# Kernel optimization log

Hardware: AMD Instinct MI355X
Metric: run time of the kernel (lower is better)

The kernel has to match this reference:

```python
import jax, jax.numpy as jnp
import numpy as np

B, N, C = 4, 2048, 1024
H = 16
D = C // H  # head dim = 64

def setup_inputs() -> dict:
    key = jax.random.key(0)
    k1, k2, k3 = jax.random.split(key, 3)
    x = jax.random.normal(k1, (B, N, C), dtype=jnp.float32)
    w_attn = jax.random.normal(k2, (C, 3 * C), dtype=jnp.float32) * (C ** -0.5)
    w_proj = jax.random.normal(k3, (C, C), dtype=jnp.float32) * (C ** -0.5)
    return {"x": x, "w_attn": w_attn, "w_proj": w_proj}

def reference(x, w_attn, w_proj):
    # fused QKV projection (bias=False)
    qkv = jnp.einsum('bnc,cf->bnf', x, w_attn)            # [B,N,3C]
    q, k, v = jnp.split(qkv, 3, axis=-1)                  # each [B,N,C]
    # [B,H,N,D]
    q = q.reshape(B, N, H, D).transpose(0, 2, 1, 3)
    k = k.reshape(B, N, H, D).transpose(0, 2, 1, 3)
    v = v.reshape(B, N, H, D).transpose(0, 2, 1, 3)
    # scaled dot-product attention, non-causal, no mask, dropout_p=0
    scale = 1.0 / jnp.sqrt(jnp.asarray(D, dtype=q.dtype))
    scores = jnp.einsum('bhqd,bhkd->bhqk', q, k) * scale  # [B,H,N,N]
    attn = jax.nn.softmax(scores, axis=-1)
    y = jnp.einsum('bhqk,bhkd->bhqd', attn, v)            # [B,H,N,D]
    y = y.transpose(0, 2, 1, 3).reshape(B, N, C)
    # output projection (bias=False); resid dropout is identity at p=0
    return jnp.einsum('bnc,co->bno', y, w_proj)
```

## Files before the change

### kernel.cpp

```cpp
#include <hip/hip_runtime.h>
#include <hip/hip_bf16.h>

typedef __hip_bfloat16 bf16;
typedef short short8 __attribute__((ext_vector_type(8)));
typedef float f32x4 __attribute__((ext_vector_type(4)));
typedef float f32x16 __attribute__((ext_vector_type(16)));

#define GLOBAL_AS __attribute__((address_space(1)))
#define LDS_AS __attribute__((address_space(3)))

__device__ inline unsigned short f2bf(float x) {
    union { float f; unsigned u; } v; v.f = x;
    unsigned r = v.u + 0x7fffu + ((v.u >> 16) & 1u);
    return (unsigned short)(r >> 16);
}

__device__ inline unsigned pkbf(float a, float b) {
    float2 f; f.x = a; f.y = b;
    union { __hip_bfloat162 h; unsigned u; } c;
    c.h = __float22bfloat162_rn(f);
    return c.u;
}

__device__ inline float fast_exp2(float x) {
#if __has_builtin(__builtin_amdgcn_exp2f)
    return __builtin_amdgcn_exp2f(x);
#else
    return exp2f(x);
#endif
}

__device__ inline void async16(const void* g, void* l) {
    __builtin_amdgcn_global_load_lds((const GLOBAL_AS void*)g, (LDS_AS void*)l, 16, 0, 0);
}


__global__ __launch_bounds__(256) void cvt_f32_bf16(const float* __restrict__ in,
                                                    unsigned short* __restrict__ out, int n4) {
    int i = blockIdx.x * 256 + threadIdx.x;
    if (i < n4) {
        float4 v = ((const float4*)in)[i];
        ushort4 o;
        o.x = f2bf(v.x); o.y = f2bf(v.y); o.z = f2bf(v.z); o.w = f2bf(v.w);
        ((ushort4*)out)[i] = o;
    }
}

__global__ __launch_bounds__(256) void transpose_bf16(const float* __restrict__ in,
                                                      unsigned short* __restrict__ out,
                                                      int R, int Cc) {
    __shared__ float s[32][33];
    int tx = threadIdx.x & 31, ty = threadIdx.x >> 5;
    int c0 = blockIdx.x * 32, r0 = blockIdx.y * 32;
#pragma unroll
    for (int i = 0; i < 4; i++)
        s[ty + i * 8][tx] = in[(size_t)(r0 + ty + i * 8) * Cc + c0 + tx];
    __syncthreads();
#pragma unroll
    for (int i = 0; i < 4; i++)
        out[(size_t)(c0 + ty + i * 8) * R + r0 + tx] = f2bf(s[tx][ty + i * 8]);
}


template <int MODE>
__global__ __launch_bounds__(256) void gemm_bf16(const bf16* __restrict__ A,
                                                 const bf16* __restrict__ Bt,
                                                 unsigned short* __restrict__ outQ,
                                                 unsigned short* __restrict__ outK,
                                                 unsigned short* __restrict__ outV,
                                                 float* __restrict__ outF, float qscale) {
    const int KD = 1024;
    __shared__ __align__(16) char smem[34816];
    bf16* sA = (bf16*)smem;
    bf16* sB = (bf16*)(smem + 16384);
    const int t = threadIdx.x;
    const int w = t >> 6, lane = t & 63, l15 = lane & 15, qd = lane >> 4;
    const int bn = blockIdx.x, bm = blockIdx.y;
    const int wm = (w >> 1) * 64, wn = (w & 1) * 64;
    const int sw = l15 & 7;

    f32x4 acc[4][4];
#pragma unroll
    for (int i = 0; i < 4; i++)
#pragma unroll
        for (int j = 0; j < 4; j++) acc[i][j] = (f32x4){0.f, 0.f, 0.f, 0.f};

    const int rsub = lane >> 3;
    const int csrc = ((lane & 7) ^ rsub) << 3;
    const bf16* Ab = A + (size_t)(bm * 128 + w * 32 + rsub) * KD + csrc;
    const bf16* Bb = Bt + (size_t)(bn * 128 + w * 32 + rsub) * KD + csrc;
    bf16* sAw = sA + (w * 32) * 64;
    bf16* sBw = sB + (w * 32) * 64;

    for (int kt = 0; kt < 16; ++kt) {
#pragma unroll
        for (int j = 0; j < 4; ++j) {
            async16(Ab + (size_t)(j * 8) * KD + kt * 64, sAw + j * 512);
            async16(Bb + (size_t)(j * 8) * KD + kt * 64, sBw + j * 512);
        }
        __syncthreads();
#pragma unroll
        for (int ks = 0; ks < 2; ++ks) {
            const int cphys = (((ks * 4 + qd) ^ sw) << 3);
            short8 af[4], bfv[4];
#pragma unroll
            for (int mi = 0; mi < 4; mi++)
                af[mi] = *(const short8*)&sA[(wm + mi * 16 + l15) * 64 + cphys];
#pragma unroll
            for (int ni = 0; ni < 4; ni++)
                bfv[ni] = *(const short8*)&sB[(wn + ni * 16 + l15) * 64 + cphys];
#pragma unroll
            for (int mi = 0; mi < 4; mi++)
#pragma unroll
                for (int ni = 0; ni < 4; ni++)
                    acc[mi][ni] = __builtin_amdgcn_mfma_f32_16x16x32_bf16(af[mi], bfv[ni],
                                                                          acc[mi][ni], 0, 0, 0);
        }
        __syncthreads();
    }

    if (MODE == 0) {
        unsigned short* sC = (unsigned short*)smem;
        const int part = bn >> 3;
        const int hb = (bn & 7) * 2;
        if (part < 2) {
            const float sc = (part == 0) ? qscale : 1.0f;
            unsigned short* dst = (part == 0) ? outQ : outK;
#pragma unroll
            for (int mi = 0; mi < 4; mi++)
#pragma unroll
                for (int ni = 0; ni < 4; ni++)
#pragma unroll
                    for (int r = 0; r < 4; r++)
                        sC[(wm + mi * 16 + qd * 4 + r) * 136 + wn + ni * 16 + l15] =
                            f2bf(acc[mi][ni][r] * sc);
            __syncthreads();
#pragma unroll
            for (int i = 0; i < 8; i++) {
                const int j = t + i * 256;
                const int row = j >> 4, c16 = j & 15;
                uint4 v = *(const uint4*)&sC[row * 136 + c16 * 8];
                const int m = bm * 128 + row;
                const int b = m >> 11, ns = m & 2047;
                const int h = hb + (c16 >> 3);
                const int dd = (c16 & 7) * 8;
                *(uint4*)&dst[((size_t)(b * 16 + h) * 2048 + ns) * 64 + dd] = v;
            }
        } else {
#pragma unroll
            for (int ni = 0; ni < 4; ni++)
#pragma unroll
                for (int mi = 0; mi < 4; mi++) {
                    uint2 pk;
                    pk.x = (unsigned)f2bf(acc[mi][ni][0]) | ((unsigned)f2bf(acc[mi][ni][1]) << 16);
                    pk.y = (unsigned)f2bf(acc[mi][ni][2]) | ((unsigned)f2bf(acc[mi][ni][3]) << 16);
                    *(uint2*)&sC[(wn + ni * 16 + l15) * 136 + wm + mi * 16 + qd * 4] = pk;
                }
            __syncthreads();
            const int m0b = bm * 128;
            const int b = m0b >> 11, ns0 = m0b & 2047;
#pragma unroll
            for (int i = 0; i < 8; i++) {
                const int j = t + i * 256;
                const int f = j >> 4, tc = j & 15;
                uint4 v = *(const uint4*)&sC[f * 136 + tc * 8];
                const int h = hb + (f >> 6), dd = f & 63;
                *(uint4*)&outV[((size_t)(b * 16 + h) * 64 + dd) * 2048 + ns0 + tc * 8] = v;
            }
        }
    } else {
        float* sF = (float*)smem;
#pragma unroll
        for (int pass = 0; pass < 2; ++pass) {
            if (pass) __syncthreads();
            if ((wm >> 6) == pass) {
#pragma unroll
                for (int mi = 0; mi < 4; mi++)
#pragma unroll
                    for (int ni = 0; ni < 4; ni++)
#pragma unroll
                        for (int r = 0; r < 4; r++)
                            sF[(mi * 16 + qd * 4 + r) * 132 + wn + ni * 16 + l15] =
                                acc[mi][ni][r];
            }
            __syncthreads();
#pragma unroll
            for (int i = 0; i < 8; i++) {
                const int j = t + i * 256;
                const int row = j >> 5, c4 = j & 31;
                float4 v = *(const float4*)&sF[row * 132 + c4 * 4];
                *(float4*)&outF[(size_t)(bm * 128 + pass * 64 + row) * 1024 + bn * 128 +
                                c4 * 4] = v;
            }
        }
    }
}


__global__ __launch_bounds__(256) void attn_kernel(const bf16* __restrict__ Q,
                                                   const bf16* __restrict__ K,
                                                   const bf16* __restrict__ Vt,
                                                   bf16* __restrict__ Y) {
    const int blk = blockIdx.x;
    const int bh = (blk & 7) * 8 + (blk >> 7);
    const int qt = (blk >> 3) & 15;
    const int b = bh >> 4, h16 = bh & 15;
    const int t = threadIdx.x, w = t >> 6, lane = t & 63;
    const int c = lane & 31, hl = lane >> 5;
    const int sw = c & 7;

    __shared__ __align__(16) char smem[32768];
    bf16* sK = (bf16*)smem;
    bf16* sVt = (bf16*)(smem + 16384);
    bf16* sO = (bf16*)smem;

    const size_t bhbase = (size_t)bh * 2048 * 64;

    short8 qf[4];
#pragma unroll
    for (int kc = 0; kc < 4; kc++)
        qf[kc] = *(const short8*)(Q + bhbase + (size_t)(qt * 128 + w * 32 + c) * 64 +
                                  kc * 16 + hl * 8);

    f32x16 ot[2];
#pragma unroll
    for (int i = 0; i < 16; i++) { ot[0][i] = 0.f; ot[1][i] = 0.f; }
    float l_run = 0.f;

    const int rsub = lane >> 3;
    const bf16* Kb = K + bhbase + (size_t)(w * 32 + rsub) * 64 + (((lane & 7) ^ rsub) << 3);
    bf16* sKw = sK + (w * 32) * 64;
    const int dsub = lane >> 4, cch = lane & 15;
    const bf16* Vb = Vt + bhbase;

    for (int kt = 0; kt < 16; ++kt) {
#pragma unroll
        for (int j = 0; j < 4; ++j)
            async16(Kb + (size_t)kt * 8192 + j * 512, sKw + j * 512);
#pragma unroll
        for (int j = 0; j < 4; ++j) {
            const int d = w * 16 + j * 4 + dsub;
            async16(Vb + (size_t)d * 2048 + kt * 128 + ((cch ^ (d & 7)) << 3),
                    sVt + (w * 16 + j * 4) * 128);
        }
        __syncthreads();

#pragma unroll
        for (int kt2 = 0; kt2 < 4; ++kt2) {
            f32x16 accS;
#pragma unroll
            for (int i = 0; i < 16; i++) accS[i] = 0.f;
#pragma unroll
            for (int kc = 0; kc < 4; kc++) {
                short8 kf =
                    *(const short8*)&sK[(kt2 * 32 + c) * 64 + (((kc * 2 + hl) ^ sw) << 3)];
                accS = __builtin_amdgcn_mfma_f32_32x32x16_bf16(kf, qf[kc], accS, 0, 0, 0);
            }
            unsigned u[8];
            float ls = 0.f;
#pragma unroll
            for (int i = 0; i < 8; i++) {
                float p0 = fast_exp2(accS[2 * i]);
                float p1 = fast_exp2(accS[2 * i + 1]);
                ls += p0 + p1;
                u[i] = pkbf(p0, p1);
            }
            l_run += ls;
            union { uint4 u4; short8 s8; } F[2];
            F[0].u4.x = u[0]; F[0].u4.y = u[1]; F[0].u4.z = u[2]; F[0].u4.w = u[3];
            F[1].u4.x = u[4]; F[1].u4.y = u[5]; F[1].u4.z = u[6]; F[1].u4.w = u[7];
#pragma unroll
            for (int g = 0; g < 2; ++g) {
#pragma unroll
                for (int mi2 = 0; mi2 < 2; mi2++) {
                    const bf16* vr = &sVt[(mi2 * 32 + c) * 128];
                    uint2 a0 = *(const uint2*)&vr[(((kt2 * 4 + 2 * g) ^ sw) << 3) + hl * 4];
                    uint2 a1 =
                        *(const uint2*)&vr[(((kt2 * 4 + 2 * g + 1) ^ sw) << 3) + hl * 4];
                    union { uint4 u4; short8 s8; } vf;
                    vf.u4.x = a0.x; vf.u4.y = a0.y; vf.u4.z = a1.x; vf.u4.w = a1.y;
                    ot[mi2] =
                        __builtin_amdgcn_mfma_f32_32x32x16_bf16(vf.s8, F[g].s8, ot[mi2], 0, 0, 0);
                }
            }
        }
        __syncthreads();
    }

    float l = l_run + __shfl_xor(l_run, 32, 64);
    float rl = 1.f / l;
#pragma unroll
    for (int mi2 = 0; mi2 < 2; mi2++)
#pragma unroll
        for (int q4 = 0; q4 < 4; q4++) {
            const int d0 = mi2 * 32 + q4 * 8 + hl * 4;
            uint2 pk;
            pk.x = pkbf(ot[mi2][q4 * 4 + 0] * rl, ot[mi2][q4 * 4 + 1] * rl);
            pk.y = pkbf(ot[mi2][q4 * 4 + 2] * rl, ot[mi2][q4 * 4 + 3] * rl);
            *(uint2*)&sO[(w * 32 + c) * 72 + d0] = pk;
        }
    __syncthreads();
#pragma unroll
    for (int i = 0; i < 4; i++) {
        int row = (t >> 3) + i * 32, doff = (t & 7) * 8;
        uint4 vv = *(const uint4*)&sO[row * 72 + doff];
        *(uint4*)(Y + ((size_t)(b * 2048 + qt * 128 + row)) * 1024 + h16 * 64 + doff) = vv;
    }
}


extern "C" void kernel_launch(void* const* d_in, const int* in_sizes, int n_in,
                              void* d_out, int out_size, void* d_ws, size_t ws_size,
                              hipStream_t stream) {
    const float* x = (const float*)d_in[0];
    const float* w_attn = (const float*)d_in[1];
    const float* w_proj = (const float*)d_in[2];
    float* out = (float*)d_out;
    char* ws = (char*)d_ws;

    bf16* xb = (bf16*)(ws);
    bf16* waT = (bf16*)(ws + 16777216);
    bf16* wpT = (bf16*)(ws + 23068672);
    bf16* qb = (bf16*)(ws + 25165824);
    bf16* kb = (bf16*)(ws + 41943040);
    bf16* vtb = (bf16*)(ws + 58720256);

    cvt_f32_bf16<<<8192, 256, 0, stream>>>(x, (unsigned short*)xb, 2097152);
    transpose_bf16<<<dim3(96, 32), 256, 0, stream>>>(w_attn, (unsigned short*)waT, 1024, 3072);
    transpose_bf16<<<dim3(32, 32), 256, 0, stream>>>(w_proj, (unsigned short*)wpT, 1024, 1024);

    const float qscale = 0.125f * 1.44269504088896340736f;
    gemm_bf16<0><<<dim3(24, 64), 256, 0, stream>>>(xb, waT, (unsigned short*)qb,
                                                   (unsigned short*)kb, (unsigned short*)vtb,
                                                   nullptr, qscale);
    attn_kernel<<<dim3(1024), 256, 0, stream>>>(qb, kb, vtb, xb );
    gemm_bf16<1><<<dim3(8, 64), 256, 0, stream>>>(xb, wpT, nullptr, nullptr, nullptr, out, 1.0f);
}
```

Measured before the change: 279.5 us.

## Double-buffer K/V tiles in attention kernel to overlap loads with compute

The attention kernel now splits shared memory into two K and two V buffers of 64 keys each and prefetches the next tile asynchronously while computing on the current one. Before, it loaded a 128-key tile and then waited on a barrier with no overlap. The aim is to hide global-to-LDS latency behind the MFMA work. In exchange, the smaller tiles double the number of barriers per query block.

```diff
diff --git a/kernel.cpp b/kernel.cpp
--- a/kernel.cpp
+++ b/kernel.cpp
@@ -210,8 +210,10 @@
     const int sw = c & 7;
 
     __shared__ __align__(16) char smem[32768];
-    bf16* sK = (bf16*)smem;
-    bf16* sVt = (bf16*)(smem + 16384);
+    bf16* sK0 = (bf16*)smem;
+    bf16* sK1 = (bf16*)(smem + 8192);
+    bf16* sV0 = (bf16*)(smem + 16384);
+    bf16* sV1 = (bf16*)(smem + 24576);
     bf16* sO = (bf16*)smem;
 
     const size_t bhbase = (size_t)bh * 2048 * 64;
@@ -228,32 +230,30 @@
     float l_run = 0.f;
 
     const int rsub = lane >> 3;
-    const bf16* Kb = K + bhbase + (size_t)(w * 32 + rsub) * 64 + (((lane & 7) ^ rsub) << 3);
-    bf16* sKw = sK + (w * 32) * 64;
-    const int dsub = lane >> 4, cch = lane & 15;
-    const bf16* Vb = Vt + bhbase;
-
-    for (int kt = 0; kt < 16; ++kt) {
-#pragma unroll
-        for (int j = 0; j < 4; ++j)
-            async16(Kb + (size_t)kt * 8192 + j * 512, sKw + j * 512);
-#pragma unroll
-        for (int j = 0; j < 4; ++j) {
-            const int d = w * 16 + j * 4 + dsub;
-            async16(Vb + (size_t)d * 2048 + kt * 128 + ((cch ^ (d & 7)) << 3),
-                    sVt + (w * 16 + j * 4) * 128);
-        }
-        __syncthreads();
-
-#pragma unroll
-        for (int kt2 = 0; kt2 < 4; ++kt2) {
+    const int cg = ((lane & 7) ^ rsub) << 3;
+    const bf16* Kb = K + bhbase + (size_t)(w * 16 + rsub) * 64 + cg;
+    const bf16* Vb = Vt + bhbase + (size_t)(w * 16 + rsub) * 2048 + cg;
+    const int ldsoff = (w * 16) * 64;
+
+#define STAGE(ktile, sKb, sVb)                                                      \
+    {                                                                               \
+        _Pragma("unroll") for (int j = 0; j < 2; j++) {                             \
+            async16(Kb + (size_t)(ktile) * 4096 + j * 512, (sKb) + ldsoff + j * 512); \
+            async16(Vb + (size_t)(ktile) * 64 + (size_t)j * 16384,                  \
+                    (sVb) + ldsoff + j * 512);                                      \
+        }                                                                           \
+    }
+
+    auto compute = [&](const bf16* __restrict__ sKb, const bf16* __restrict__ sVb) {
+#pragma unroll
+        for (int kt2 = 0; kt2 < 2; ++kt2) {
             f32x16 accS;
 #pragma unroll
             for (int i = 0; i < 16; i++) accS[i] = 0.f;
 #pragma unroll
             for (int kc = 0; kc < 4; kc++) {
                 short8 kf =
-                    *(const short8*)&sK[(kt2 * 32 + c) * 64 + (((kc * 2 + hl) ^ sw) << 3)];
+                    *(const short8*)&sKb[(kt2 * 32 + c) * 64 + (((kc * 2 + hl) ^ sw) << 3)];
                 accS = __builtin_amdgcn_mfma_f32_32x32x16_bf16(kf, qf[kc], accS, 0, 0, 0);
             }
             unsigned u[8];
@@ -273,7 +273,7 @@
             for (int g = 0; g < 2; ++g) {
 #pragma unroll
                 for (int mi2 = 0; mi2 < 2; mi2++) {
-                    const bf16* vr = &sVt[(mi2 * 32 + c) * 128];
+                    const bf16* vr = &sVb[(mi2 * 32 + c) * 64];
                     uint2 a0 = *(const uint2*)&vr[(((kt2 * 4 + 2 * g) ^ sw) << 3) + hl * 4];
                     uint2 a1 =
                         *(const uint2*)&vr[(((kt2 * 4 + 2 * g + 1) ^ sw) << 3) + hl * 4];
@@ -284,8 +284,18 @@
                 }
             }
         }
+    };
+
+    STAGE(0, sK0, sV0);
+    for (int kt = 0; kt < 32; kt += 2) {
         __syncthreads();
-    }
+        STAGE(kt + 1, sK1, sV1);
+        compute(sK0, sV0);
+        __syncthreads();
+        if (kt + 2 < 32) STAGE(kt + 2, sK0, sV0);
+        compute(sK1, sV1);
+    }
+    __syncthreads();
 
     float l = l_run + __shfl_xor(l_run, 32, 64);
     float rl = 1.f / l;
@@ -306,6 +316,7 @@
         uint4 vv = *(const uint4*)&sO[row * 72 + doff];
         *(uint4*)(Y + ((size_t)(b * 2048 + qt * 128 + row)) * 1024 + h16 * 64 + doff) = vv;
     }
+#undef STAGE
 }
 
 
```

After: 275.9 us. Within noise of the previous version (-1.3%).
